# Optimization experiments

Hardware: AMD Instinct MI355X
Metric: run time of the kernel (lower is better)

## Reference

```python
import jax, jax.numpy as jnp
import numpy as np

N = 64          # Hilbert space dim
B = 4096        # batch of density matrices
K = 2           # number of jump operators
DT = 0.01       # time step
C = (0.0, 0.5, 1.0)
A = ((0.0, 0.0, 0.0), (0.5, 0.0, 0.0), (0.0, 1.0, 0.0))
BW = (1.0 / 6.0, 2.0 / 3.0, 1.0 / 6.0)
NEUMANN_ORDER = 2


def _dag(M):
    # real-valued reference: dagger == transpose on last two axes
    return jnp.swapaxes(M, -1, -2)


def _sandwich(M, rho):
    # M rho M^dag ; M:[N,N], rho:[B,N,N]
    return M @ rho @ _dag(M)


def _dissipator(L, rho):
    # sum_k L_k rho L_k^dag ; L:[K,N,N], rho:[B,N,N]
    return jnp.einsum('kij,bjl,kml->bim', L, rho, L)


def _neumann_ratio(Ui, Uj, I):
    # U(ci) U(cj)^{-1} with U(cj)^{-1} ~ sum_{p<=order} (I - U(cj))^p
    W = I - Uj
    inv = I
    Wp = I
    for _ in range(NEUMANN_ORDER):
        Wp = Wp @ W
        inv = inv + Wp
    return Ui @ inv


def _forward(rho0, U_half, U_one, L0, Lh, L1):
    I = jnp.eye(N, dtype=rho0.dtype)
    Umap = {0.0: I, 0.5: U_half, 1.0: U_one}
    Lmap = {0.0: L0, 0.5: Lh, 1.0: L1}

    def ratio(ci, cj):
        if ci == cj:
            return I
        if cj == 0.0:
            return Umap[ci]
        return _neumann_ratio(Umap[ci], Umap[cj], I)

    # intermediate stages rho^(i)
    stages = []
    for i, ci in enumerate(C):
        rho_i = rho0 if ci == 0.0 else _sandwich(Umap[ci], rho0)
        for j in range(i):
            a_ij = A[i][j]
            if a_ij == 0.0:
                continue
            cj = C[j]
            P_ij = ratio(ci, cj)
            rho_i = rho_i + DT * a_ij * _sandwich(P_ij, _dissipator(Lmap[cj], stages[j]))
        stages.append(rho_i)

    # output combination
    rho_new = _sandwich(Umap[1.0], rho0)
    for i, bi in enumerate(BW):
        if bi == 0.0:
            continue
        ci = C[i]
        Q_i = ratio(1.0, ci)
        rho_new = rho_new + DT * bi * _sandwich(Q_i, _dissipator(Lmap[ci], stages[i]))
    return rho_new


def setup_inputs() -> dict:
    key = jax.random.key(0)
    k1, k2, k3, k4, k5, k6 = jax.random.split(key, 6)
    I = jnp.eye(N, dtype=jnp.float32)
    rho0 = jax.random.normal(k1, (B, N, N), dtype=jnp.float32)
    rho0 = 0.5 * (rho0 + jnp.swapaxes(rho0, -1, -2))  # hermitian-like
    # no-jump propagators: near-identity so the Neumann series is sane
    U_half = I + 0.02 * jax.random.normal(k2, (N, N), dtype=jnp.float32)
    U_one = I + 0.04 * jax.random.normal(k3, (N, N), dtype=jnp.float32)
    L0 = 0.1 * jax.random.normal(k4, (K, N, N), dtype=jnp.float32)
    Lh = 0.1 * jax.random.normal(k5, (K, N, N), dtype=jnp.float32)
    L1 = 0.1 * jax.random.normal(k6, (K, N, N), dtype=jnp.float32)
    return {"rho0": rho0, "U_half": U_half, "U_one": U_one,
            "L0": L0, "Lh": Lh, "L1": L1}


def reference(rho0, U_half, U_one, L0, Lh, L1):
    return _forward(rho0, U_half, U_one, L0, Lh, L1)
```

## Files before the change

kernel.cpp:

```cpp
#include <hip/hip_runtime.h>
#include <hip/hip_bf16.h>

#define NDIM 64
#define BP   72
#define DT_  0.01f
#define NTERM 7

typedef __attribute__((ext_vector_type(8)))  short bf16x8;
typedef __attribute__((ext_vector_type(16))) float f32x16;

struct Frag { bf16x8 f[4]; };


__device__ __forceinline__ unsigned short f2b(float x) {
    __hip_bfloat16 h = __float2bfloat16(x);
    return __builtin_bit_cast(unsigned short, h);
}
__device__ __forceinline__ float b2f(unsigned short u) {
    unsigned int v = (unsigned int)u << 16;
    return __builtin_bit_cast(float, v);
}
__device__ __forceinline__ unsigned int f2b2(float lo, float hi) {
    return (unsigned int)f2b(lo) | ((unsigned int)f2b(hi) << 16);
}


__device__ __forceinline__ bf16x8 ldfrag(const unsigned short* M, int rb, int j, int ln, int hq) {
    return *(const bf16x8*)&M[(rb + ln) * BP + j * 16 + hq * 8];
}

__device__ __forceinline__ void ldg_op(Frag& F, const unsigned short* __restrict__ p,
                                       int ln, int hq, int cw) {
#pragma unroll
    for (int j = 0; j < 4; ++j)
        F.f[j] = *(const bf16x8*)&p[(cw + ln) * 64 + j * 16 + hq * 8];
}

__device__ __forceinline__ void ldsF(Frag& F, const unsigned short* p, int ln, int hq, int cw) {
#pragma unroll
    for (int j = 0; j < 4; ++j)
        F.f[j] = *(const bf16x8*)&p[(cw + ln) * BP + j * 16 + hq * 8];
}

__device__ __forceinline__ void ldg_opF32(Frag& F, const float* __restrict__ P,
                                          int ln, int hq, int cw) {
    const int n = cw + ln;
#pragma unroll
    for (int j = 0; j < 4; ++j) {
        const float* q = &P[n * 64 + j * 16 + hq * 8];
        float4 u = *(const float4*)q;
        float4 v = *(const float4*)(q + 4);
        uint4 o;
        o.x = f2b2(u.x, u.y); o.y = f2b2(u.z, u.w);
        o.z = f2b2(v.x, v.y); o.w = f2b2(v.z, v.w);
        F.f[j] = __builtin_bit_cast(bf16x8, o);
    }
}

__device__ __forceinline__ void ldWfrag(Frag& F, const float* __restrict__ Uh,
                                        int ln, int hq, int cw) {
    const int n = cw + ln;
#pragma unroll
    for (int j = 0; j < 4; ++j) {
        const int k0 = j * 16 + hq * 8;
        const float* q = &Uh[n * 64 + k0];
        float4 u = *(const float4*)q;
        float4 v = *(const float4*)(q + 4);
        float wv[8] = {-u.x, -u.y, -u.z, -u.w, -v.x, -v.y, -v.z, -v.w};
#pragma unroll
        for (int e = 0; e < 8; ++e)
            if (n == k0 + e) wv[e] += 1.f;
        uint4 o;
        o.x = f2b2(wv[0], wv[1]); o.y = f2b2(wv[2], wv[3]);
        o.z = f2b2(wv[4], wv[5]); o.w = f2b2(wv[6], wv[7]);
        F.f[j] = __builtin_bit_cast(bf16x8, o);
    }
}

template <bool ACC>
__device__ __forceinline__ void ntg(const unsigned short* A, const Frag& F, f32x16& acc,
                                    int ln, int hq, int rb) {
    if (!ACC) {
#pragma unroll
        for (int r = 0; r < 16; ++r) acc[r] = 0.f;
    }
#pragma unroll
    for (int j = 0; j < 4; ++j)
        acc = __builtin_amdgcn_mfma_f32_32x32x16_bf16(ldfrag(A, rb, j, ln, hq), F.f[j], acc, 0, 0, 0);
}

__device__ __forceinline__ f32x16 ntg_reg(const Frag& A, const Frag& F, const f32x16& Z) {
    f32x16 a = __builtin_amdgcn_mfma_f32_32x32x16_bf16(A.f[0], F.f[0], Z, 0, 0, 0);
#pragma unroll
    for (int j = 1; j < 4; ++j)
        a = __builtin_amdgcn_mfma_f32_32x32x16_bf16(A.f[j], F.f[j], a, 0, 0, 0);
    return a;
}

__device__ __forceinline__ void stT(unsigned short* D, const f32x16& v,
                                    int ln, int hq, int rw, int cw) {
#pragma unroll
    for (int g = 0; g < 4; ++g) {
        uint2 o;
        o.x = f2b2(v[4 * g + 0], v[4 * g + 1]);
        o.y = f2b2(v[4 * g + 2], v[4 * g + 3]);
        *(uint2*)&D[(cw + ln) * BP + rw + 8 * g + 4 * hq] = o;
    }
}

__device__ __forceinline__ void stN(unsigned short* D, const f32x16& v,
                                    int ln, int hq, int rw, int cw) {
#pragma unroll
    for (int r = 0; r < 16; ++r) {
        int row = rw + (r & 3) + 8 * (r >> 2) + 4 * hq;
        D[row * BP + (cw + ln)] = f2b(v[r]);
    }
}

__device__ __forceinline__ void ldT(float* r, const unsigned short* S,
                                    int ln, int hq, int rw, int cw) {
#pragma unroll
    for (int g = 0; g < 4; ++g) {
        uint2 u = *(const uint2*)&S[(cw + ln) * BP + rw + 8 * g + 4 * hq];
        unsigned short o[4];
        *(uint2*)o = u;
#pragma unroll
        for (int j = 0; j < 4; ++j) r[4 * g + j] = b2f(o[j]);
    }
}

__device__ __forceinline__ void emit(unsigned short* __restrict__ g, const f32x16& v, float s,
                                     int ln, int hq, int rw, int cw) {
#pragma unroll
    for (int gq = 0; gq < 4; ++gq) {
        uint2 o;
        o.x = f2b2(s * v[4 * gq + 0], s * v[4 * gq + 1]);
        o.y = f2b2(s * v[4 * gq + 2], s * v[4 * gq + 3]);
        *(uint2*)&g[(cw + ln) * 64 + rw + 8 * gq + 4 * hq] = o;
    }
}


__global__ void __launch_bounds__(256) krk_setup(const float* __restrict__ Uh,
                                                 const float* __restrict__ U1,
                                                 const float* __restrict__ L0,
                                                 const float* __restrict__ Lh,
                                                 const float* __restrict__ L1,
                                                 unsigned short* __restrict__ ws) {
    __shared__ unsigned short B[7][NDIM * BP];

    const int tid = threadIdx.x;
    const int lane = tid & 63, w = tid >> 6, ln = lane & 31, hq = lane >> 5;
    const int rw = 32 * (w >> 1), cw = 32 * (w & 1);

    const float c16 = DT_ / 6.f, c23 = 2.f * DT_ / 3.f;
    const float sA = sqrtf(c16);
    const float sB = sqrtf(c23);

#pragma unroll
    for (int i = 0; i < 4; ++i) {
        int flat = (tid + i * 256) * 4;
        int r = flat >> 6, c = flat & 63;
        float4 u = *(const float4*)&Uh[flat];
        const float* uf = (const float*)&u;
        float wv[4];
#pragma unroll
        for (int j = 0; j < 4; ++j) wv[j] = ((r == c + j) ? 1.f : 0.f) - uf[j];
#pragma unroll
        for (int j = 0; j < 4; ++j) B[0][(c + j) * BP + r] = f2b(uf[j]);
        uint2 ow; ow.x = f2b2(wv[0], wv[1]); ow.y = f2b2(wv[2], wv[3]);
        *(uint2*)&B[4][r * BP + c] = ow;
#pragma unroll
        for (int j = 0; j < 4; ++j) B[5][(c + j) * BP + r] = f2b(wv[j]);

        float4 p = *(const float4*)&U1[flat];
        const float* pf = (const float*)&p;
#pragma unroll
        for (int j = 0; j < 4; ++j) B[1][(c + j) * BP + r] = f2b(pf[j]);
        uint2 oq; oq.x = f2b2(p.x, p.y); oq.y = f2b2(p.z, p.w);
        *(uint2*)&ws[flat] = oq;

        float4 a = *(const float4*)&L0[flat];
        const float* af = (const float*)&a;
#pragma unroll
        for (int j = 0; j < 4; ++j) B[2][(c + j) * BP + r] = f2b(af[j]);
        float4 b = *(const float4*)&L0[4096 + flat];
        const float* bf = (const float*)&b;
#pragma unroll
        for (int j = 0; j < 4; ++j) B[3][(c + j) * BP + r] = f2b(bf[j]);
    }

    Frag FUh, FU1, FLh0, FLh1, F10, F11, Fw;
    ldg_opF32(FUh,  Uh,        ln, hq, cw);
    ldg_opF32(FU1,  U1,        ln, hq, cw);
    ldg_opF32(FLh0, Lh,        ln, hq, cw);
    ldg_opF32(FLh1, Lh + 4096, ln, hq, cw);
    ldg_opF32(F10,  L1,        ln, hq, cw);
    ldg_opF32(F11,  L1 + 4096, ln, hq, cw);
    ldWfrag(Fw, Uh, ln, hq, cw);
    __syncthreads();

    f32x16 e;

    {
        f32x16 t0;
        ntg<false>(B[5], Fw, t0, ln, hq, rw);
        float wts[16];
        ldT(wts, B[4], ln, hq, rw, cw);
#pragma unroll
        for (int g = 0; g < 4; ++g) {
            float vv[4];
#pragma unroll
            for (int i = 0; i < 4; ++i) {
                int r = 4 * g + i;
                int row = rw + i + 8 * g + 4 * hq;
                vv[i] = ((row == cw + ln) ? 1.f : 0.f) + wts[r] + t0[r];
            }
            uint2 o; o.x = f2b2(vv[0], vv[1]); o.y = f2b2(vv[2], vv[3]);
            *(uint2*)&B[6][(cw + ln) * BP + rw + 8 * g + 4 * hq] = o;
        }
    }
    ntg<false>(B[2], FU1, e, ln, hq, rw); emit(ws + 1 * 4096, e, sA, ln, hq, rw, cw);
    ntg<false>(B[3], FU1, e, ln, hq, rw); emit(ws + 2 * 4096, e, sA, ln, hq, rw, cw);
    ntg<false>(B[1], F10, e, ln, hq, rw); emit(ws + 5 * 4096, e, sA, ln, hq, rw, cw);
    ntg<false>(B[1], F11, e, ln, hq, rw); emit(ws + 6 * 4096, e, sA, ln, hq, rw, cw);
    __syncthreads();

    Frag FV; ldsF(FV, B[6], ln, hq, cw);

    ntg<false>(B[0], FLh0, e, ln, hq, rw); stN(B[2], e, ln, hq, rw, cw);
    ntg<false>(B[0], FLh1, e, ln, hq, rw); stN(B[3], e, ln, hq, rw, cw);
    __syncthreads();

    ntg<false>(B[2], FV, e, ln, hq, rw); stN(B[4], e, ln, hq, rw, cw);
    ntg<false>(B[3], FV, e, ln, hq, rw); stN(B[5], e, ln, hq, rw, cw);
    __syncthreads();

    ntg<false>(B[4], FU1, e, ln, hq, rw); emit(ws + 3 * 4096, e, sB, ln, hq, rw, cw);
    ntg<false>(B[5], FU1, e, ln, hq, rw); emit(ws + 4 * 4096, e, sB, ln, hq, rw, cw);
}


__global__ void __launch_bounds__(256, 2) krk_main(const float* __restrict__ rho0,
                                                   const unsigned short* __restrict__ ws,
                                                   float* __restrict__ out) {
    __shared__ unsigned short S[4][2][NDIM * BP];

    const int tid = threadIdx.x;
    const int w = tid >> 6, lane = tid & 63, ln = lane & 31, hq = lane >> 5;
    const int rw = 32 * (w >> 1), cw = 32 * (w & 1);

    Frag Ar[4];
#pragma unroll
    for (int m = 0; m < 4; ++m) {
        const float* rho = rho0 + (size_t)(4 * blockIdx.x + m) * 4096;
        const float* q0 = &rho[(rw + ln) * 64];
#pragma unroll
        for (int j = 0; j < 4; ++j) {
            const float* q = q0 + j * 16 + hq * 8;
            float4 u = *(const float4*)q;
            float4 v = *(const float4*)(q + 4);
            uint4 o;
            o.x = f2b2(u.x, u.y); o.y = f2b2(u.z, u.w);
            o.z = f2b2(v.x, v.y); o.w = f2b2(v.z, v.w);
            Ar[m].f[j] = __builtin_bit_cast(bf16x8, o);
        }
    }

    f32x16 Z;
#pragma unroll
    for (int r = 0; r < 16; ++r) Z[r] = 0.f;
    f32x16 acc[4] = {Z, Z, Z, Z};

    Frag F[2];
    ldg_op(F[0], ws, ln, hq, cw);

#pragma unroll
    for (int t = 0; t < NTERM; ++t) {
        if (t > 0) {
#pragma unroll
            for (int m = 0; m < 4; ++m)
                ntg<true>(S[m][(t - 1) & 1], F[(t - 1) & 1], acc[m], ln, hq, rw);
        }
#pragma unroll
        for (int m = 0; m < 4; ++m) {
            f32x16 tv = ntg_reg(Ar[m], F[t & 1], Z);
            stT(S[m][t & 1], tv, ln, hq, rw, cw);
        }
        if (t + 1 < NTERM)
            ldg_op(F[(t + 1) & 1], ws + (size_t)(t + 1) * 4096, ln, hq, cw);
        __syncthreads();
    }

#pragma unroll
    for (int m = 0; m < 4; ++m) {
        ntg<true>(S[m][(NTERM - 1) & 1], F[(NTERM - 1) & 1], acc[m], ln, hq, rw);
        float* o = out + (size_t)(4 * blockIdx.x + m) * 4096;
#pragma unroll
        for (int g = 0; g < 4; ++g) {
            float4 v;
            v.x = acc[m][4 * g + 0];
            v.y = acc[m][4 * g + 1];
            v.z = acc[m][4 * g + 2];
            v.w = acc[m][4 * g + 3];
            *(float4*)&o[(cw + ln) * 64 + rw + 8 * g + 4 * hq] = v;
        }
    }
}


extern "C" void kernel_launch(void* const* d_in, const int* in_sizes, int n_in,
                              void* d_out, int out_size, void* d_ws, size_t ws_size,
                              hipStream_t stream) {
    const float* rho0 = (const float*)d_in[0];
    const float* Uh   = (const float*)d_in[1];
    const float* U1   = (const float*)d_in[2];
    const float* L0   = (const float*)d_in[3];
    const float* Lh   = (const float*)d_in[4];
    const float* L1   = (const float*)d_in[5];
    float* out = (float*)d_out;
    unsigned short* ws = (unsigned short*)d_ws;

    int Bn = in_sizes[0] / (NDIM * NDIM);

    krk_setup<<<1, 256, 0, stream>>>(Uh, U1, L0, Lh, L1, ws);
    krk_main<<<Bn / 4, 256, 0, stream>>>(rho0, ws, out);
}
```

Measured before the change: 155.1 us.

## Compute each matrix per wave in registers using permlane32 swaps instead of LDS

Each wave now owns one whole 64x64 density matrix instead of four waves sharing four matrices through shared memory. The intermediate product M·rho is converted to bf16 and rearranged into MFMA A-operand fragments with v_permlane32_swap, so no LDS staging or __syncthreads is needed. This removes LDS traffic and barriers, at the cost of more registers per wave (four accumulators plus two operand fragment sets), which could lower occupancy.

```diff
diff --git a/kernel.cpp b/kernel.cpp
--- a/kernel.cpp
+++ b/kernel.cpp
@@ -22,6 +22,10 @@
 }
 __device__ __forceinline__ unsigned int f2b2(float lo, float hi) {
     return (unsigned int)f2b(lo) | ((unsigned int)f2b(hi) << 16);
+}
+
+__device__ __forceinline__ void plswap(unsigned int& a, unsigned int& b) {
+    asm("v_permlane32_swap_b32 %0, %1" : "+v"(a), "+v"(b));
 }
 
 
@@ -95,17 +99,6 @@
     for (int j = 1; j < 4; ++j)
         a = __builtin_amdgcn_mfma_f32_32x32x16_bf16(A.f[j], F.f[j], a, 0, 0, 0);
     return a;
-}
-
-__device__ __forceinline__ void stT(unsigned short* D, const f32x16& v,
-                                    int ln, int hq, int rw, int cw) {
-#pragma unroll
-    for (int g = 0; g < 4; ++g) {
-        uint2 o;
-        o.x = f2b2(v[4 * g + 0], v[4 * g + 1]);
-        o.y = f2b2(v[4 * g + 2], v[4 * g + 3]);
-        *(uint2*)&D[(cw + ln) * BP + rw + 8 * g + 4 * hq] = o;
-    }
 }
 
 __device__ __forceinline__ void stN(unsigned short* D, const f32x16& v,
@@ -244,68 +237,82 @@
 __global__ void __launch_bounds__(256, 2) krk_main(const float* __restrict__ rho0,
                                                    const unsigned short* __restrict__ ws,
                                                    float* __restrict__ out) {
-    __shared__ unsigned short S[4][2][NDIM * BP];
-
     const int tid = threadIdx.x;
     const int w = tid >> 6, lane = tid & 63, ln = lane & 31, hq = lane >> 5;
-    const int rw = 32 * (w >> 1), cw = 32 * (w & 1);
-
-    Frag Ar[4];
-#pragma unroll
-    for (int m = 0; m < 4; ++m) {
-        const float* rho = rho0 + (size_t)(4 * blockIdx.x + m) * 4096;
-        const float* q0 = &rho[(rw + ln) * 64];
+
+    const int mat = 4 * blockIdx.x + w;
+    const float* rho = rho0 + (size_t)mat * 4096;
+
+    Frag Ar[2];
+#pragma unroll
+    for (int kb = 0; kb < 2; ++kb)
 #pragma unroll
         for (int j = 0; j < 4; ++j) {
-            const float* q = q0 + j * 16 + hq * 8;
+            const float* q = &rho[(kb * 32 + ln) * 64 + j * 16 + hq * 8];
             float4 u = *(const float4*)q;
             float4 v = *(const float4*)(q + 4);
             uint4 o;
             o.x = f2b2(u.x, u.y); o.y = f2b2(u.z, u.w);
             o.z = f2b2(v.x, v.y); o.w = f2b2(v.z, v.w);
-            Ar[m].f[j] = __builtin_bit_cast(bf16x8, o);
-        }
-    }
+            Ar[kb].f[j] = __builtin_bit_cast(bf16x8, o);
+        }
 
     f32x16 Z;
 #pragma unroll
     for (int r = 0; r < 16; ++r) Z[r] = 0.f;
-    f32x16 acc[4] = {Z, Z, Z, Z};
-
-    Frag F[2];
-    ldg_op(F[0], ws, ln, hq, cw);
+    f32x16 acc00 = Z, acc01 = Z, acc10 = Z, acc11 = Z;
+
+    Frag F[2][2];
+    ldg_op(F[0][0], ws, ln, hq, 0);
+    ldg_op(F[0][1], ws, ln, hq, 32);
 
 #pragma unroll
     for (int t = 0; t < NTERM; ++t) {
-        if (t > 0) {
-#pragma unroll
-            for (int m = 0; m < 4; ++m)
-                ntg<true>(S[m][(t - 1) & 1], F[(t - 1) & 1], acc[m], ln, hq, rw);
-        }
-#pragma unroll
-        for (int m = 0; m < 4; ++m) {
-            f32x16 tv = ntg_reg(Ar[m], F[t & 1], Z);
-            stT(S[m][t & 1], tv, ln, hq, rw, cw);
-        }
-        if (t + 1 < NTERM)
-            ldg_op(F[(t + 1) & 1], ws + (size_t)(t + 1) * 4096, ln, hq, cw);
-        __syncthreads();
-    }
-
-#pragma unroll
-    for (int m = 0; m < 4; ++m) {
-        ntg<true>(S[m][(NTERM - 1) & 1], F[(NTERM - 1) & 1], acc[m], ln, hq, rw);
-        float* o = out + (size_t)(4 * blockIdx.x + m) * 4096;
-#pragma unroll
-        for (int g = 0; g < 4; ++g) {
-            float4 v;
-            v.x = acc[m][4 * g + 0];
-            v.y = acc[m][4 * g + 1];
-            v.z = acc[m][4 * g + 2];
-            v.w = acc[m][4 * g + 3];
-            *(float4*)&o[(cw + ln) * 64 + rw + 8 * g + 4 * hq] = v;
-        }
-    }
+        const int cur = t & 1, nxt = cur ^ 1;
+        if (t + 1 < NTERM) {
+            ldg_op(F[nxt][0], ws + (size_t)(t + 1) * 4096, ln, hq, 0);
+            ldg_op(F[nxt][1], ws + (size_t)(t + 1) * 4096, ln, hq, 32);
+        }
+#pragma unroll
+        for (int c = 0; c < 2; ++c) {
+            Frag afr;
+#pragma unroll
+            for (int kb = 0; kb < 2; ++kb) {
+                f32x16 T = ntg_reg(Ar[kb], F[cur][c], Z);
+                unsigned int P[8];
+#pragma unroll
+                for (int p = 0; p < 8; ++p) P[p] = f2b2(T[2 * p], T[2 * p + 1]);
+                plswap(P[0], P[2]); plswap(P[1], P[3]);
+                plswap(P[4], P[6]); plswap(P[5], P[7]);
+                uint4 lo; lo.x = P[0]; lo.y = P[1]; lo.z = P[2]; lo.w = P[3];
+                uint4 hi; hi.x = P[4]; hi.y = P[5]; hi.z = P[6]; hi.w = P[7];
+                afr.f[2 * kb]     = __builtin_bit_cast(bf16x8, lo);
+                afr.f[2 * kb + 1] = __builtin_bit_cast(bf16x8, hi);
+            }
+#pragma unroll
+            for (int j = 0; j < 4; ++j) {
+                f32x16& a0 = c ? acc10 : acc00;
+                f32x16& a1 = c ? acc11 : acc01;
+                a0 = __builtin_amdgcn_mfma_f32_32x32x16_bf16(afr.f[j], F[cur][0].f[j], a0, 0, 0, 0);
+                a1 = __builtin_amdgcn_mfma_f32_32x32x16_bf16(afr.f[j], F[cur][1].f[j], a1, 0, 0, 0);
+            }
+        }
+    }
+
+    float* o = out + (size_t)mat * 4096;
+#pragma unroll
+    for (int I = 0; I < 2; ++I)
+#pragma unroll
+        for (int J = 0; J < 2; ++J) {
+            const f32x16& a = I ? (J ? acc11 : acc10) : (J ? acc01 : acc00);
+#pragma unroll
+            for (int g = 0; g < 4; ++g) {
+                float4 v;
+                v.x = a[4 * g + 0]; v.y = a[4 * g + 1];
+                v.z = a[4 * g + 2]; v.w = a[4 * g + 3];
+                *(float4*)&o[(J * 32 + ln) * 64 + I * 32 + 8 * g + 4 * hq] = v;
+            }
+        }
 }
 
 
```

Result: slower. 161.6 us (+4.2%).
